# Kernel tuning notes

Hardware: AMD Instinct MI355X
Metric: run time of the kernel (lower is better)

Reference implementation:

```python
import jax, jax.numpy as jnp
import numpy as np

BETA = 0.025
K, D = 8192, 256
B, T = 32, 1024

def setup_inputs() -> dict:
    key = jax.random.key(0)
    k1, k2 = jax.random.split(key)
    z_e = jax.random.normal(k1, (B, T, D), dtype=jnp.float32)
    # variance_scaling(scale=1, mode='fan_avg', distribution='uniform') over (K, D)
    fan_avg = (K + D) / 2.0
    limit = np.sqrt(3.0 / fan_avg)
    codebook = jax.random.uniform(k2, (K, D), dtype=jnp.float32, minval=-limit, maxval=limit)
    return {"z_e": z_e, "codebook": codebook}

def reference(z_e, codebook):
    flat = z_e.reshape(-1, D)  # [N, D]
    x_sqr = jnp.sum(flat ** 2, axis=-1, keepdims=True)        # [N, 1]
    c_sqr = jnp.sum(codebook ** 2, axis=-1)[None, :]           # [1, K]
    distances = x_sqr - 2.0 * (flat @ codebook.T) + c_sqr      # [N, K]
    encoding_indices = jnp.argmin(distances, axis=-1).reshape(z_e.shape[:-1])  # [B, T]
    quantize = codebook[encoding_indices]                      # [B, T, D]
    encoding_loss = jnp.mean((jax.lax.stop_gradient(z_e) - quantize) ** 2)
    commitment_loss = jnp.mean((z_e - jax.lax.stop_gradient(quantize)) ** 2)
    loss = encoding_loss + BETA * commitment_loss
    z_q = z_e + jax.lax.stop_gradient(quantize - z_e)          # straight-through
    return (z_q, encoding_indices, loss)
```

## Files before the change

### kernel.cpp

```cpp
#include <hip/hip_runtime.h>

#define D     256
#define K     8192
#define NROWS 32768
#define BETA  0.025f
#define TAU_NEW 2e-3f
#define TAU_OLD 2e-4f

typedef _Float16 f16x8 __attribute__((ext_vector_type(8)));
typedef unsigned short ushort8v __attribute__((ext_vector_type(8)));
typedef float f32x16 __attribute__((ext_vector_type(16)));

#define MFMAH(a,b,c) __builtin_amdgcn_mfma_f32_32x32x16_f16(a,b,c,0,0,0)

typedef __attribute__((address_space(3))) unsigned int lds_uint;
typedef __attribute__((address_space(1))) unsigned int glb_uint;
__device__ __forceinline__ void gld16(const void* g, void* l) {
    __builtin_amdgcn_global_load_lds((const glb_uint*)g, (lds_uint*)l, 16, 0, 0);
}

__global__ __launch_bounds__(256)
void np_sumsq_kernel(const float* __restrict__ src, float* __restrict__ dst,
                     int nrows) {
    const int tid  = threadIdx.x;
    const int w    = tid >> 6;
    const int lane = tid & 63;
    const int row  = blockIdx.x * 4 + w;
    if (row >= nrows) return;
    const float* a = src + (size_t)row * D;
    float r = 0.0f;
    if (lane < 16) {
        const float* h = a + (lane >> 3) * 128;
        const int j = lane & 7;
        float v = h[j];
        r = __fmul_rn(v, v);
        #pragma unroll
        for (int i = 8; i < 128; i += 8) {
            float u = h[i + j];
            r = __fadd_rn(r, __fmul_rn(u, u));
        }
    }
    float rr[16];
    #pragma unroll
    for (int t = 0; t < 16; ++t) rr[t] = __shfl(r, t, 64);
    if (lane == 0) {
        float h0 = __fadd_rn(__fadd_rn(__fadd_rn(rr[0], rr[1]), __fadd_rn(rr[2], rr[3])),
                             __fadd_rn(__fadd_rn(rr[4], rr[5]), __fadd_rn(rr[6], rr[7])));
        float h1 = __fadd_rn(__fadd_rn(__fadd_rn(rr[8], rr[9]), __fadd_rn(rr[10], rr[11])),
                             __fadd_rn(__fadd_rn(rr[12], rr[13]), __fadd_rn(rr[14], rr[15])));
        dst[row] = __fadd_rn(h0, h1);
    }
}

__global__ __launch_bounds__(64)
void np_sumsq_flagged_kernel(const float* __restrict__ ze,
                             const int* __restrict__ nflag,
                             const int* __restrict__ flags,
                             float* __restrict__ x2, int cap) {
    const int lane = threadIdx.x;
    const int nf   = min(nflag[0], cap);
    for (int f = blockIdx.x; f < nf; f += gridDim.x) {
        const int row = flags[f];
        const float* a = ze + (size_t)row * D;
        float r = 0.0f;
        if (lane < 16) {
            const float* h = a + (lane >> 3) * 128;
            const int j = lane & 7;
            float v = h[j];
            r = __fmul_rn(v, v);
            #pragma unroll
            for (int i = 8; i < 128; i += 8) {
                float u = h[i + j];
                r = __fadd_rn(r, __fmul_rn(u, u));
            }
        }
        float rr[16];
        #pragma unroll
        for (int t = 0; t < 16; ++t) rr[t] = __shfl(r, t, 64);
        if (lane == 0) {
            float h0 = __fadd_rn(__fadd_rn(__fadd_rn(rr[0], rr[1]), __fadd_rn(rr[2], rr[3])),
                                 __fadd_rn(__fadd_rn(rr[4], rr[5]), __fadd_rn(rr[6], rr[7])));
            float h1 = __fadd_rn(__fadd_rn(__fadd_rn(rr[8], rr[9]), __fadd_rn(rr[10], rr[11])),
                                 __fadd_rn(__fadd_rn(rr[12], rr[13]), __fadd_rn(rr[14], rr[15])));
            x2[row] = __fadd_rn(h0, h1);
        }
    }
}

__global__ __launch_bounds__(256)
void pack_cb_kernel(const float* __restrict__ cb, unsigned short* __restrict__ cbp) {
    const int t  = blockIdx.x;
    const int l  = threadIdx.x & 63;
    const int cq = threadIdx.x >> 6;
    const int row = t * 32 + (l & 31);
    const int db  = 8 * (l >> 5);
    #pragma unroll
    for (int ci = 0; ci < 4; ++ci) {
        const int c  = cq * 4 + ci;
        const int d0 = c * 16 + db;
        float4 v0 = *reinterpret_cast<const float4*>(&cb[(size_t)row * D + d0]);
        float4 v1 = *reinterpret_cast<const float4*>(&cb[(size_t)row * D + d0 + 4]);
        float xv[8] = {v0.x, v0.y, v0.z, v0.w, v1.x, v1.y, v1.z, v1.w};
        f16x8 hv;
        #pragma unroll
        for (int j = 0; j < 8; ++j) hv[j] = (_Float16)xv[j];
        *reinterpret_cast<f16x8*>(cbp + (((size_t)t * 16 + c) * 64 + l) * 8) = hv;
    }
}

__global__ __launch_bounds__(256)
void mfma_argmin_kernel(const float* __restrict__ ze,
                        const unsigned short* __restrict__ cbp,
                        const float* __restrict__ c2,
                        float2* __restrict__ tops, int* __restrict__ topi) {
    __shared__ unsigned short lds[2 * 8192];
    const int tid = threadIdx.x;
    const int l   = tid & 63;
    const int w   = tid >> 6;
    const int ks  = blockIdx.x & 1;
    const int nb  = blockIdx.x >> 1;
    const int n   = nb * 128 + w * 32 + (l & 31);
    const int h   = l >> 5;

    f16x8 Bf[16];
    {
        const float* zr = ze + (size_t)n * D + 8 * h;
        #pragma unroll
        for (int c = 0; c < 16; ++c) {
            float4 v0 = *reinterpret_cast<const float4*>(zr + c * 16);
            float4 v1 = *reinterpret_cast<const float4*>(zr + c * 16 + 4);
            float xv[8] = {v0.x, v0.y, v0.z, v0.w, v1.x, v1.y, v1.z, v1.w};
            f16x8 hv;
            #pragma unroll
            for (int j = 0; j < 8; ++j) hv[j] = (_Float16)xv[j];
            Bf[c] = hv;
        }
    }

    const int t0 = ks * 128;
    const uint4* gsrc = reinterpret_cast<const uint4*>(cbp);

    auto stage = [&](int t, int buf) {
        const uint4* g = gsrc + (size_t)t * 1024 + w * 256 + l;
        uint4* lb = reinterpret_cast<uint4*>(lds + buf * 8192) + w * 256;
        #pragma unroll
        for (int r = 0; r < 4; ++r)
            gld16(g + r * 64, lb + r * 64);
    };

    stage(t0, 0);
    __builtin_amdgcn_sched_barrier(0);
    __syncthreads();

    float b1 = 3.4e38f, b2 = 3.4e38f;
    int   i1 = 0;
    int   cur = 0;

    for (int ti = 0; ti < 128; ++ti) {
        const int t = t0 + ti;
        if (ti + 1 < 128) stage(t + 1, cur ^ 1);
        __builtin_amdgcn_sched_barrier(0);

        const uint4* abuf = reinterpret_cast<const uint4*>(lds + cur * 8192);
        f32x16 a0, a1;
        #pragma unroll
        for (int i = 0; i < 16; ++i) { a0[i] = 0.0f; a1[i] = 0.0f; }
        #pragma unroll
        for (int c = 0; c < 16; c += 2) {
            f16x8 A0 = __builtin_bit_cast(f16x8, abuf[(c + 0) * 64 + l]);
            f16x8 A1 = __builtin_bit_cast(f16x8, abuf[(c + 1) * 64 + l]);
            a0 = MFMAH(A0, Bf[c + 0], a0);
            a1 = MFMAH(A1, Bf[c + 1], a1);
        }
        const float* c2t = c2 + t * 32 + 4 * h;
        const int base = t * 32 + 4 * h;
        #pragma unroll
        for (int g = 0; g < 4; ++g) {
            float4 cv = *reinterpret_cast<const float4*>(c2t + 8 * g);
            #pragma unroll
            for (int q = 0; q < 4; ++q) {
                const int reg = g * 4 + q;
                float dot = a0[reg] + a1[reg];
                float cc  = (q == 0) ? cv.x : (q == 1) ? cv.y : (q == 2) ? cv.z : cv.w;
                float s   = fmaf(-2.0f, dot, cc);
                int code  = base + 8 * g + q;
                bool lt = s < b1;
                b2 = fminf(b2, lt ? b1 : s);
                i1 = lt ? code : i1;
                b1 = lt ? s : b1;
            }
        }
        __syncthreads();
        cur ^= 1;
    }

    float ob1 = __shfl_xor(b1, 32);
    float ob2 = __shfl_xor(b2, 32);
    int   oi1 = __shfl_xor(i1, 32);
    bool take = (ob1 < b1) || (ob1 == b1 && oi1 < i1);
    float nb2 = fminf(fmaxf(b1, ob1), fminf(b2, ob2));
    float nb1 = take ? ob1 : b1;
    int   ni1 = take ? oi1 : i1;
    if (l < 32) {
        tops[(size_t)n * 2 + ks] = make_float2(nb1, nb2);
        topi[(size_t)n * 2 + ks] = ni1;
    }
}

__global__ __launch_bounds__(256)
void ksplit_merge_kernel(const float2* __restrict__ tops, const int* __restrict__ topi,
                         int* __restrict__ idx_out, float* __restrict__ idxf_out,
                         int* __restrict__ nflag, int* __restrict__ flags, float tau) {
    const int n = blockIdx.x * 256 + threadIdx.x;
    float2 e0 = tops[(size_t)n * 2 + 0];
    float2 e1 = tops[(size_t)n * 2 + 1];
    int    i0 = topi[(size_t)n * 2 + 0];
    int    i1v = topi[(size_t)n * 2 + 1];
    bool take = (e1.x < e0.x) || (e1.x == e0.x && i1v < i0);
    float b1 = take ? e1.x : e0.x;
    int   bi = take ? i1v : i0;
    float b2 = fminf(fmaxf(e0.x, e1.x), fminf(e0.y, e1.y));
    idx_out[n]  = bi;
    idxf_out[n] = (float)bi;
    if (b2 - b1 < tau) {
        int p = atomicAdd(nflag, 1);
        flags[p] = n;
    }
}

__global__ __launch_bounds__(256)
void fix1_kernel(const float* __restrict__ ze, const float* __restrict__ cb,
                 const float* __restrict__ c2, const float* __restrict__ x2,
                 const int* __restrict__ nflag, const int* __restrict__ flags,
                 float* __restrict__ scr_s, int* __restrict__ scr_i, int cap) {
    __shared__ float sz[D];
    __shared__ float sbest[16];
    __shared__ int   sbi[16];
    const int tid     = threadIdx.x;
    const int cl      = tid >> 4;
    const int dt      = tid & 15;
    const int cbblk   = blockIdx.x & 511;
    const int stripe  = blockIdx.x >> 9;
    const int nstripe = gridDim.x >> 9;
    const int code    = cbblk * 16 + cl;
    const int nf      = min(nflag[0], cap);
    if (nf == 0) return;
    double cbr[16];
    {
        const float* crp = cb + (size_t)code * D + dt;
        #pragma unroll
        for (int j = 0; j < 16; ++j) cbr[j] = (double)crp[16 * j];
    }
    const float cc = c2[code];
    for (int f = stripe; f < nf; f += nstripe) {
        const int row = flags[f];
        __syncthreads();
        sz[tid] = ze[(size_t)row * D + tid];
        __syncthreads();
        double dot = 0.0;
        #pragma unroll
        for (int j = 0; j < 16; ++j)
            dot = fma((double)sz[dt + 16 * j], cbr[j], dot);
        #pragma unroll
        for (int o = 1; o < 16; o <<= 1)
            dot += __shfl_xor(dot, o);
        if (dt == 0) {
            float P  = (float)dot;
            float t3 = __fadd_rn(x2[row], __fmul_rn(-2.0f, P));
            float t4 = __fadd_rn(t3, cc);
            sbest[cl] = t4; sbi[cl] = code;
        }
        __syncthreads();
        if (tid == 0) {
            float bs = sbest[0]; int bi = sbi[0];
            #pragma unroll
            for (int c = 1; c < 16; ++c)
                if (sbest[c] < bs) { bs = sbest[c]; bi = sbi[c]; }
            scr_s[(size_t)f * 512 + cbblk] = bs;
            scr_i[(size_t)f * 512 + cbblk] = bi;
        }
    }
}

__global__ __launch_bounds__(256)
void fix2_kernel(const int* __restrict__ nflag, const int* __restrict__ flags,
                 const float* __restrict__ scr_s, const int* __restrict__ scr_i,
                 int* __restrict__ idx_out, float* __restrict__ idxf_out, int cap) {
    __shared__ float ss[256];
    __shared__ int   si[256];
    const int tid = threadIdx.x;
    const int nf  = min(nflag[0], cap);
    for (int f = blockIdx.x; f < nf; f += gridDim.x) {
        float s0 = scr_s[(size_t)f * 512 + tid];
        int   j0 = scr_i[(size_t)f * 512 + tid];
        float s1 = scr_s[(size_t)f * 512 + 256 + tid];
        int   j1 = scr_i[(size_t)f * 512 + 256 + tid];
        bool take = (s1 < s0) || (s1 == s0 && j1 < j0);
        ss[tid] = take ? s1 : s0;
        si[tid] = take ? j1 : j0;
        __syncthreads();
        for (int o = 128; o; o >>= 1) {
            if (tid < o) {
                if (ss[tid + o] < ss[tid] ||
                    (ss[tid + o] == ss[tid] && si[tid + o] < si[tid])) {
                    ss[tid] = ss[tid + o]; si[tid] = si[tid + o];
                }
            }
            __syncthreads();
        }
        if (tid == 0) {
            const int row = flags[f];
            idx_out[row]  = si[0];
            idxf_out[row] = (float)si[0];
        }
        __syncthreads();
    }
}

__global__ __launch_bounds__(512)
void argmin_fp32_kernel(const float* __restrict__ ze, const float* __restrict__ cb,
                        const float* __restrict__ c2,
                        int* __restrict__ idx_out, float* __restrict__ idxf_out,
                        int* __restrict__ nflag, int* __restrict__ flags) {
    __shared__ float smem[12672];
    float* a_s = smem;
    float* b_s = smem + 32 * 128;
    const int tid  = threadIdx.x;
    const int tx   = tid & 31;
    const int ty   = tid >> 5;
    const int row0 = blockIdx.x * 128;
    float b1[8], b2[8];
    int   i1[8];
    #pragma unroll
    for (int r = 0; r < 8; ++r) { b1[r] = 3.4e38f; b2[r] = 3.4e38f; i1[r] = 0; }
    for (int kt = 0; kt < K; kt += 256) {
        float acc[8][8];
        #pragma unroll
        for (int r = 0; r < 8; ++r)
            #pragma unroll
            for (int c = 0; c < 8; ++c) acc[r][c] = 0.0f;
        for (int dc = 0; dc < D; dc += 32) {
            __syncthreads();
            #pragma unroll
            for (int j = 0; j < 2; ++j) {
                int p = tid + j * 512, ar = p >> 3, ad = (p & 7) << 2;
                float4 v = *reinterpret_cast<const float4*>(&ze[(size_t)(row0 + ar) * D + dc + ad]);
                a_s[(ad + 0) * 128 + ar] = v.x; a_s[(ad + 1) * 128 + ar] = v.y;
                a_s[(ad + 2) * 128 + ar] = v.z; a_s[(ad + 3) * 128 + ar] = v.w;
            }
            #pragma unroll
            for (int j = 0; j < 4; ++j) {
                int p = tid + j * 512, br = p >> 3, bd = (p & 7) << 2;
                float4 v = *reinterpret_cast<const float4*>(&cb[(size_t)(kt + br) * D + dc + bd]);
                b_s[(bd + 0) * 256 + br] = v.x; b_s[(bd + 1) * 256 + br] = v.y;
                b_s[(bd + 2) * 256 + br] = v.z; b_s[(bd + 3) * 256 + br] = v.w;
            }
            __syncthreads();
            #pragma unroll 4
            for (int d = 0; d < 32; ++d) {
                float4 a0  = *reinterpret_cast<const float4*>(&a_s[d * 128 + ty * 4]);
                float4 a1  = *reinterpret_cast<const float4*>(&a_s[d * 128 + 64 + ty * 4]);
                float4 b0  = *reinterpret_cast<const float4*>(&b_s[d * 256 + tx * 4]);
                float4 b1v = *reinterpret_cast<const float4*>(&b_s[d * 256 + 128 + tx * 4]);
                float av[8] = {a0.x, a0.y, a0.z, a0.w, a1.x, a1.y, a1.z, a1.w};
                float bv[8] = {b0.x, b0.y, b0.z, b0.w, b1v.x, b1v.y, b1v.z, b1v.w};
                #pragma unroll
                for (int r = 0; r < 8; ++r)
                    #pragma unroll
                    for (int c = 0; c < 8; ++c)
                        acc[r][c] = fmaf(av[r], bv[c], acc[r][c]);
            }
        }
        float4 cs0 = *reinterpret_cast<const float4*>(&c2[kt + tx * 4]);
        float4 cs1 = *reinterpret_cast<const float4*>(&c2[kt + 128 + tx * 4]);
        float cv[8] = {cs0.x, cs0.y, cs0.z, cs0.w, cs1.x, cs1.y, cs1.z, cs1.w};
        #pragma unroll
        for (int r = 0; r < 8; ++r)
            #pragma unroll
            for (int c = 0; c < 8; ++c) {
                int col = kt + ((c < 4) ? (tx * 4 + c) : (128 + tx * 4 + (c - 4)));
                float s = fmaf(-2.0f, acc[r][c], cv[c]);
                if (s < b1[r]) { b2[r] = b1[r]; b1[r] = s; i1[r] = col; }
                else if (s < b2[r]) { b2[r] = s; }
            }
    }
    __syncthreads();
    float* rs1 = smem;
    int*   ri  = (int*)(smem + 4224);
    float* rs2 = smem + 8448;
    #pragma unroll
    for (int r = 0; r < 8; ++r) {
        int lrow = (r >> 2) * 64 + ty * 4 + (r & 3);
        rs1[lrow * 33 + tx] = b1[r]; ri[lrow * 33 + tx] = i1[r]; rs2[lrow * 33 + tx] = b2[r];
    }
    __syncthreads();
    if (tid < 128) {
        float B1 = 3.4e38f, B2 = 3.4e38f;
        int I1 = 0;
        #pragma unroll 4
        for (int t = 0; t < 32; ++t) {
            float s1 = rs1[tid * 33 + t]; int j1 = ri[tid * 33 + t]; float s2 = rs2[tid * 33 + t];
            if (s1 < B1 || (s1 == B1 && j1 < I1)) { B2 = fminf(B2, B1); B1 = s1; I1 = j1; }
            else B2 = fminf(B2, s1);
            B2 = fminf(B2, s2);
        }
        int grow = row0 + tid;
        idx_out[grow] = I1;
        idxf_out[grow] = (float)I1;
        if (B2 - B1 < TAU_OLD) { int p = atomicAdd(nflag, 1); flags[p] = grow; }
    }
}

__global__ __launch_bounds__(256)
void fix_old_kernel(const float* __restrict__ ze, const float* __restrict__ cb,
                    const float* __restrict__ c2, const float* __restrict__ x2,
                    const int* __restrict__ nflag, const int* __restrict__ flags,
                    int* __restrict__ idx_out, float* __restrict__ idxf_out) {
    __shared__ __align__(16) float sx[D];
    __shared__ float sbest[256];
    __shared__ int   sidx[256];
    const int tid = threadIdx.x;
    const int n   = nflag[0];
    for (int f = blockIdx.x; f < n; f += gridDim.x) {
        __syncthreads();
        const int row = flags[f];
        sx[tid] = ze[(size_t)row * D + tid];
        const float x2r = x2[row];
        __syncthreads();
        const float4* sx4 = reinterpret_cast<const float4*>(sx);
        float best = 3.4e38f; int bi = K;
        for (int k = tid; k < K; k += 256) {
            const float4* cbr = reinterpret_cast<const float4*>(&cb[(size_t)k * D]);
            double dot = 0.0;
            #pragma unroll 8
            for (int d4 = 0; d4 < D / 4; ++d4) {
                float4 c = cbr[d4]; float4 x = sx4[d4];
                dot = fma((double)x.x, (double)c.x, dot);
                dot = fma((double)x.y, (double)c.y, dot);
                dot = fma((double)x.z, (double)c.z, dot);
                dot = fma((double)x.w, (double)c.w, dot);
            }
            float P  = (float)dot;
            float t3 = __fadd_rn(x2r, __fmul_rn(-2.0f, P));
            float t4 = __fadd_rn(t3, c2[k]);
            if (t4 < best || (t4 == best && k < bi)) { best = t4; bi = k; }
        }
        sbest[tid] = best; sidx[tid] = bi;
        __syncthreads();
        for (int o = 128; o; o >>= 1) {
            if (tid < o) {
                if (sbest[tid + o] < sbest[tid] ||
                    (sbest[tid + o] == sbest[tid] && sidx[tid + o] < sidx[tid])) {
                    sbest[tid] = sbest[tid + o]; sidx[tid] = sidx[tid + o];
                }
            }
            __syncthreads();
        }
        if (tid == 0) { idx_out[row] = sidx[0]; idxf_out[row] = (float)sidx[0]; }
    }
}

__global__ __launch_bounds__(256)
void gather_loss_kernel(const float* __restrict__ ze, const float* __restrict__ cb,
                        const int* __restrict__ idx, float* __restrict__ zq,
                        float* __restrict__ partial) {
    const int tid  = threadIdx.x;
    const int w    = tid >> 6;
    const int lane = tid & 63;
    const int n    = blockIdx.x * 4 + w;
    const int k    = idx[n];
    float4 q = *reinterpret_cast<const float4*>(&cb[(size_t)k * D + lane * 4]);
    float4 z = *reinterpret_cast<const float4*>(&ze[(size_t)n * D + lane * 4]);
    *reinterpret_cast<float4*>(&zq[(size_t)n * D + lane * 4]) = q;
    float dx = z.x - q.x, dy = z.y - q.y, dz = z.z - q.z, dw = z.w - q.w;
    float s = dx * dx + dy * dy + dz * dz + dw * dw;
    #pragma unroll
    for (int o = 32; o; o >>= 1) s += __shfl_down(s, o);
    __shared__ float ws4[4];
    if (lane == 0) ws4[w] = s;
    __syncthreads();
    if (tid == 0) partial[blockIdx.x] = ws4[0] + ws4[1] + ws4[2] + ws4[3];
}

__global__ __launch_bounds__(256)
void final_loss_kernel(const float* __restrict__ partial, float* __restrict__ out) {
    __shared__ float sm[256];
    const int tid = threadIdx.x;
    float s = 0.0f;
    for (int i = tid; i < 8192; i += 256) s += partial[i];
    sm[tid] = s;
    __syncthreads();
    #pragma unroll
    for (int o = 128; o; o >>= 1) {
        if (tid < o) sm[tid] += sm[tid + o];
        __syncthreads();
    }
    if (tid == 0)
        out[0] = sm[0] * (1.0f + BETA) / (float)(NROWS * D);
}

extern "C" void kernel_launch(void* const* d_in, const int* in_sizes, int n_in,
                              void* d_out, int out_size, void* d_ws, size_t ws_size,
                              hipStream_t stream) {
    const float* ze = (const float*)d_in[0];
    const float* cb = (const float*)d_in[1];

    float* out  = (float*)d_out;
    float* zq   = out;
    float* idxf = out + (size_t)NROWS * D;
    float* loss = out + (size_t)NROWS * D + NROWS;

    char* ws = (char*)d_ws;
    float*  c2      = (float*) (ws);
    float*  x2      = (float*) (ws + 32768);
    int*    idx     = (int*)   (ws + 163840);
    float*  partial = (float*) (ws + 294912);
    int*    nflag   = (int*)   (ws + 327680);
    int*    flags   = (int*)   (ws + 327696);
    float2* tops    = (float2*)(ws + 458768);
    int*    topi    = (int*)   (ws + 983056);
    unsigned short* cbp = (unsigned short*)(ws + 1245200);
    float*  scr_s   = (float*) (ws + 9633808);
    const size_t scr_base = 9633808;

    const size_t need_min = scr_base + (size_t)2048 * 4096;
    const bool newpath = ws_size >= need_min;
    int cap = 0;
    int* scr_i = nullptr;
    if (newpath) {
        size_t avail = (ws_size - scr_base) / 4096;
        cap = (int)(avail > 8192 ? 8192 : avail);
        scr_i = (int*)(ws + scr_base + (size_t)cap * 2048);
    }

    hipMemsetAsync(nflag, 0, sizeof(int), stream);
    hipLaunchKernelGGL(np_sumsq_kernel, dim3(K / 4), dim3(256), 0, stream, cb, c2, K);

    if (newpath) {
        hipLaunchKernelGGL(pack_cb_kernel,     dim3(256), dim3(256), 0, stream, cb, cbp);
        hipLaunchKernelGGL(mfma_argmin_kernel, dim3(512), dim3(256), 0, stream,
                           ze, cbp, c2, tops, topi);
        hipLaunchKernelGGL(ksplit_merge_kernel, dim3(NROWS / 256), dim3(256), 0, stream,
                           tops, topi, idx, idxf, nflag, flags, TAU_NEW);
        hipLaunchKernelGGL(np_sumsq_flagged_kernel, dim3(256), dim3(64), 0, stream,
                           ze, nflag, flags, x2, cap);
        hipLaunchKernelGGL(fix1_kernel, dim3(8192), dim3(256), 0, stream,
                           ze, cb, c2, x2, nflag, flags, scr_s, scr_i, cap);
        hipLaunchKernelGGL(fix2_kernel, dim3(128), dim3(256), 0, stream,
                           nflag, flags, scr_s, scr_i, idx, idxf, cap);
    } else {
        hipLaunchKernelGGL(argmin_fp32_kernel, dim3(NROWS / 128), dim3(512), 0, stream,
                           ze, cb, c2, idx, idxf, nflag, flags);
        hipLaunchKernelGGL(np_sumsq_flagged_kernel, dim3(128), dim3(64), 0, stream,
                           ze, nflag, flags, x2, NROWS);
        hipLaunchKernelGGL(fix_old_kernel, dim3(256), dim3(256), 0, stream,
                           ze, cb, c2, x2, nflag, flags, idx, idxf);
    }

    hipLaunchKernelGGL(gather_loss_kernel, dim3(NROWS / 4), dim3(256), 0, stream,
                       ze, cb, idx, zq, partial);
    hipLaunchKernelGGL(final_loss_kernel, dim3(1), dim3(256), 0, stream,
                       partial, loss);
}
```

Before: 439.4 us.

## Stage codebook tiles through registers and batch flagged rows in fix1

The main distance kernel stops using direct global-to-LDS loads. It prefetches the next codebook tile into registers, then writes it to the alternate LDS buffer after compute, adding a second barrier per iteration. Separately, fix1 now processes up to 8 flagged rows per barrier round instead of one, which amortizes the synchronization and the row loads. The register staging costs extra VGPRs and an extra barrier per tile, and it may interact differently with the MFMA schedule.

```diff
diff --git a/kernel.cpp b/kernel.cpp
--- a/kernel.cpp
+++ b/kernel.cpp
@@ -6,18 +6,13 @@
 #define BETA  0.025f
 #define TAU_NEW 2e-3f
 #define TAU_OLD 2e-4f
+#define RB    8
 
 typedef _Float16 f16x8 __attribute__((ext_vector_type(8)));
 typedef unsigned short ushort8v __attribute__((ext_vector_type(8)));
 typedef float f32x16 __attribute__((ext_vector_type(16)));
 
 #define MFMAH(a,b,c) __builtin_amdgcn_mfma_f32_32x32x16_f16(a,b,c,0,0,0)
-
-typedef __attribute__((address_space(3))) unsigned int lds_uint;
-typedef __attribute__((address_space(1))) unsigned int glb_uint;
-__device__ __forceinline__ void gld16(const void* g, void* l) {
-    __builtin_amdgcn_global_load_lds((const glb_uint*)g, (lds_uint*)l, 16, 0, 0);
-}
 
 __global__ __launch_bounds__(256)
 void np_sumsq_kernel(const float* __restrict__ src, float* __restrict__ dst,
@@ -140,16 +135,20 @@
     const int t0 = ks * 128;
     const uint4* gsrc = reinterpret_cast<const uint4*>(cbp);
 
-    auto stage = [&](int t, int buf) {
+    uint4 pf[4];
+    auto prefetch = [&](int t) {
         const uint4* g = gsrc + (size_t)t * 1024 + w * 256 + l;
-        uint4* lb = reinterpret_cast<uint4*>(lds + buf * 8192) + w * 256;
-        #pragma unroll
-        for (int r = 0; r < 4; ++r)
-            gld16(g + r * 64, lb + r * 64);
+        #pragma unroll
+        for (int r = 0; r < 4; ++r) pf[r] = g[r * 64];
     };
-
-    stage(t0, 0);
-    __builtin_amdgcn_sched_barrier(0);
+    auto commit = [&](int buf) {
+        uint4* lb = reinterpret_cast<uint4*>(lds + (size_t)buf * 8192) + w * 256 + l;
+        #pragma unroll
+        for (int r = 0; r < 4; ++r) lb[r * 64] = pf[r];
+    };
+
+    prefetch(t0);
+    commit(0);
     __syncthreads();
 
     float b1 = 3.4e38f, b2 = 3.4e38f;
@@ -158,10 +157,9 @@
 
     for (int ti = 0; ti < 128; ++ti) {
         const int t = t0 + ti;
-        if (ti + 1 < 128) stage(t + 1, cur ^ 1);
-        __builtin_amdgcn_sched_barrier(0);
-
-        const uint4* abuf = reinterpret_cast<const uint4*>(lds + cur * 8192);
+        if (ti + 1 < 128) prefetch(t + 1);
+
+        const uint4* abuf = reinterpret_cast<const uint4*>(lds + (size_t)cur * 8192);
         f32x16 a0, a1;
         #pragma unroll
         for (int i = 0; i < 16; ++i) { a0[i] = 0.0f; a1[i] = 0.0f; }
@@ -190,6 +188,8 @@
                 b1 = lt ? s : b1;
             }
         }
+        __syncthreads();
+        if (ti + 1 < 128) commit(cur ^ 1);
         __syncthreads();
         cur ^= 1;
     }
@@ -233,9 +233,8 @@
                  const float* __restrict__ c2, const float* __restrict__ x2,
                  const int* __restrict__ nflag, const int* __restrict__ flags,
                  float* __restrict__ scr_s, int* __restrict__ scr_i, int cap) {
-    __shared__ float sz[D];
-    __shared__ float sbest[16];
-    __shared__ int   sbi[16];
+    __shared__ float sz[RB][D];
+    __shared__ float sbest[RB][16];
     const int tid     = threadIdx.x;
     const int cl      = tid >> 4;
     const int dt      = tid & 15;
@@ -245,6 +244,8 @@
     const int code    = cbblk * 16 + cl;
     const int nf      = min(nflag[0], cap);
     if (nf == 0) return;
+    const int perStripe = (nf - stripe + nstripe - 1) / nstripe;
+    if (perStripe <= 0) return;
     double cbr[16];
     {
         const float* crp = cb + (size_t)code * D + dt;
@@ -252,32 +253,43 @@
         for (int j = 0; j < 16; ++j) cbr[j] = (double)crp[16 * j];
     }
     const float cc = c2[code];
-    for (int f = stripe; f < nf; f += nstripe) {
-        const int row = flags[f];
-        __syncthreads();
-        sz[tid] = ze[(size_t)row * D + tid];
-        __syncthreads();
-        double dot = 0.0;
-        #pragma unroll
-        for (int j = 0; j < 16; ++j)
-            dot = fma((double)sz[dt + 16 * j], cbr[j], dot);
-        #pragma unroll
-        for (int o = 1; o < 16; o <<= 1)
-            dot += __shfl_xor(dot, o);
-        if (dt == 0) {
-            float P  = (float)dot;
-            float t3 = __fadd_rn(x2[row], __fmul_rn(-2.0f, P));
-            float t4 = __fadd_rn(t3, cc);
-            sbest[cl] = t4; sbi[cl] = code;
-        }
-        __syncthreads();
-        if (tid == 0) {
-            float bs = sbest[0]; int bi = sbi[0];
+    for (int it = 0; it < perStripe; it += RB) {
+        __syncthreads();
+        #pragma unroll
+        for (int r = 0; r < RB; ++r) {
+            if (it + r < perStripe) {
+                const int row = flags[stripe + nstripe * (it + r)];
+                sz[r][tid] = ze[(size_t)row * D + tid];
+            }
+        }
+        __syncthreads();
+        #pragma unroll
+        for (int r = 0; r < RB; ++r) {
+            if (it + r < perStripe) {
+                double dot = 0.0;
+                #pragma unroll
+                for (int j = 0; j < 16; ++j)
+                    dot = fma((double)sz[r][dt + 16 * j], cbr[j], dot);
+                #pragma unroll
+                for (int o = 1; o < 16; o <<= 1)
+                    dot += __shfl_xor(dot, o);
+                if (dt == 0) {
+                    const int f = stripe + nstripe * (it + r);
+                    float P  = (float)dot;
+                    float t3 = __fadd_rn(x2[flags[f]], __fmul_rn(-2.0f, P));
+                    sbest[r][cl] = __fadd_rn(t3, cc);
+                }
+            }
+        }
+        __syncthreads();
+        if (tid < RB && it + tid < perStripe) {
+            const int f = stripe + nstripe * (it + tid);
+            float bs = sbest[tid][0]; int bc = 0;
             #pragma unroll
             for (int c = 1; c < 16; ++c)
-                if (sbest[c] < bs) { bs = sbest[c]; bi = sbi[c]; }
+                if (sbest[tid][c] < bs) { bs = sbest[tid][c]; bc = c; }
             scr_s[(size_t)f * 512 + cbblk] = bs;
-            scr_i[(size_t)f * 512 + cbblk] = bi;
+            scr_i[(size_t)f * 512 + cbblk] = cbblk * 16 + bc;
         }
     }
 }
```

Result: slower. 621.6 us (+41.5%).
